# Kernel optimization log

Hardware: AMD Instinct MI355X
Metric: run time of the kernel (lower is better)

The kernel has to match this reference:

```python
import jax, jax.numpy as jnp
import numpy as np

N, E, L, F, HID, OUT = 20000, 200000, 5, 4, 128, 3


def _lin(x, w, b):
    # torch Linear convention: w is [out, in]
    return x @ w.T + b


def setup_inputs() -> dict:
    key = jax.random.key(0)
    ks = iter(jax.random.split(key, 40))
    nrm = lambda shape, s=0.05: jax.random.normal(next(ks), shape, dtype=jnp.float32) * s
    inp = {
        'x': jax.random.normal(next(ks), (N, L, F), dtype=jnp.float32),
        'edge_index': jax.random.randint(next(ks), (2, E), 0, N, dtype=jnp.int64),
        'edge_attr': jax.random.normal(next(ks), (E, F), dtype=jnp.float32),
        'batch': jnp.zeros((N,), dtype=jnp.int64),
        'node_type': jax.random.normal(next(ks), (N, 1), dtype=jnp.float32),
        # PastStateEncoder params
        'emb': nrm((L, F), 1.0),
        'conv_w': nrm((HID, 2 * F, 3)),  # Conv1d(8,128,3) OIW
        'conv_b': nrm((HID,)),
        # FusionLayer Linear(129,128)
        'fuse_w': nrm((HID, HID + 1)), 'fuse_b': nrm((HID,)),
        # gnn1 EdgeModel: Linear(2*128+4,128), Linear(128,128)
        'g1e_w1': nrm((HID, 2 * HID + F)), 'g1e_b1': nrm((HID,)),
        'g1e_w2': nrm((HID, HID)), 'g1e_b2': nrm((HID,)),
        # gnn1 NodeModel: Linear(256,128), Linear(128,128)
        'g1n_w1': nrm((HID, 2 * HID)), 'g1n_b1': nrm((HID,)),
        'g1n_w2': nrm((HID, HID)), 'g1n_b2': nrm((HID,)),
        # gnn2 EdgeModel: Linear(2*128+128,128), Linear(128,128)
        'g2e_w1': nrm((HID, 3 * HID)), 'g2e_b1': nrm((HID,)),
        'g2e_w2': nrm((HID, HID)), 'g2e_b2': nrm((HID,)),
        # gnn2 NodeModel
        'g2n_w1': nrm((HID, 2 * HID)), 'g2n_b1': nrm((HID,)),
        'g2n_w2': nrm((HID, HID)), 'g2n_b2': nrm((HID,)),
        # final_mlp: Linear(128,128), BN(128), Linear(128,3)
        'fm_w1': nrm((HID, HID)), 'fm_b1': nrm((HID,)),
        'bn_g': jnp.ones((HID,), dtype=jnp.float32), 'bn_b': jnp.zeros((HID,), dtype=jnp.float32),
        'fm_w2': nrm((OUT, HID)), 'fm_b2': nrm((OUT,)),
    }
    return inp


def _encoder(x, emb, conv_w, conv_b):
    # x: [N, L, F]; append learned positional embedding -> [N, L, 2F]
    n = x.shape[0]
    xe = jnp.concatenate([x, jnp.broadcast_to(emb[None], (n, L, F))], axis=-1)
    xc = xe.transpose(0, 2, 1)  # [N, 2F, L]
    y = jax.lax.conv_general_dilated(
        xc, conv_w, window_strides=(1,), padding=[(1, 1)],
        dimension_numbers=('NCW', 'OIW', 'NCW'))
    y = y + conv_b[None, :, None]
    return y.mean(axis=-1)  # [N, HID]


def _edge_mlp(src, dst, ea, w1, b1, w2, b2):
    h = jax.nn.relu(_lin(jnp.concatenate([src, dst, ea], axis=1), w1, b1))
    return _lin(h, w2, b2)


def _node_mlp(x_row, ea, w1, b1, w2, b2):
    h = jax.nn.relu(_lin(jnp.concatenate([x_row, ea], axis=1), w1, b1))
    return _lin(h, w2, b2)


def reference(x, edge_index, edge_attr, batch, node_type,
              emb, conv_w, conv_b, fuse_w, fuse_b,
              g1e_w1, g1e_b1, g1e_w2, g1e_b2, g1n_w1, g1n_b1, g1n_w2, g1n_b2,
              g2e_w1, g2e_b1, g2e_w2, g2e_b2, g2n_w1, g2n_b1, g2n_w2, g2n_b2,
              fm_w1, fm_b1, bn_g, bn_b, fm_w2, fm_b2):
    row, col = edge_index[0], edge_index[1]
    h = _encoder(x, emb, conv_w, conv_b)                     # [N,128]
    h = _lin(jnp.concatenate([h, node_type], axis=-1), fuse_w, fuse_b)  # [N,128]
    # gnn1 (MetaLayer: edge model then node model; node model here is per-edge)
    ea = _edge_mlp(h[row], h[col], edge_attr, g1e_w1, g1e_b1, g1e_w2, g1e_b2)  # [E,128]
    h = _node_mlp(h[row], ea, g1n_w1, g1n_b1, g1n_w2, g1n_b2)                  # [E,128]
    # gnn2 (h now lives on edges; indices < N <= E remain valid, matching torch)
    ea = _edge_mlp(h[row], h[col], ea, g2e_w1, g2e_b1, g2e_w2, g2e_b2)
    h = _node_mlp(h[row], ea, g2n_w1, g2n_b1, g2n_w2, g2n_b2)
    # final head on edge_attr: Linear -> BatchNorm1d (training stats) -> ReLU -> Linear
    z = _lin(ea, fm_w1, fm_b1)
    mu = z.mean(axis=0)
    var = z.var(axis=0)  # biased, matches torch BN normalization
    z = (z - mu) * jax.lax.rsqrt(var + 1e-5) * bn_g + bn_b
    z = jax.nn.relu(z)
    return _lin(z, fm_w2, fm_b2)  # [E,3]
```

## Files before the change

### kernel.cpp

```cpp
#include <hip/hip_runtime.h>

#define N_NODES 20000
#define N_EDGES 200000
#define HID 128
#define STR 136
#define NBLK 3125
#define NREP 64

typedef unsigned short u16;
using bf16x8 = __attribute__((ext_vector_type(8))) __bf16;
using f32x4  = __attribute__((ext_vector_type(4))) float;

__device__ __forceinline__ u16 f2bf(float f) {
  union { float f; unsigned u; } v; v.f = f;
  unsigned u = v.u;
  return (u16)((u + 0x7FFFu + ((u >> 16) & 1u)) >> 16);
}
__device__ __forceinline__ float bf2f(unsigned s) {
  union { unsigned u; float f; } v; v.u = s << 16;
  return v.f;
}
__device__ __forceinline__ bf16x8 ld8(const u16* p) { return *(const bf16x8*)p; }

__device__ __forceinline__ void zero_acc8(f32x4 acc[4]) {
#pragma unroll
  for (int i = 0; i < 4; ++i) acc[i] = (f32x4){0.f, 0.f, 0.f, 0.f};
}

template <int KSTEPS, typename AF>
__device__ __forceinline__ void wgemm8(const u16* __restrict__ PW, AF afrag,
                                       f32x4 acc[4], int lane, int wave) {
  const u16* pb = PW + (wave * 64 + lane) * 8;
  bf16x8 b[2];
  b[0] = ld8(pb);
#pragma unroll
  for (int ks = 0; ks < KSTEPS; ++ks) {
    const int cur = ks & 1;
    if (ks + 1 < KSTEPS) b[cur ^ 1] = ld8(pb + (ks + 1) * 4096);
#pragma unroll
    for (int mt = 0; mt < 4; ++mt) {
      bf16x8 a = afrag(ks, mt);
      acc[mt] = __builtin_amdgcn_mfma_f32_16x16x32_bf16(a, b[cur], acc[mt], 0, 0, 0);
    }
  }
}

template <bool RELU>
__device__ __forceinline__ void epi_store8(u16* buf, const f32x4 acc[4],
                                           const float* __restrict__ bias,
                                           int lane, int wave) {
  const int c = lane & 15, q = lane >> 4;
  const float bb = bias[wave * 16 + c];
  const int col = wave * 16 + c;
#pragma unroll
  for (int mt = 0; mt < 4; ++mt)
#pragma unroll
    for (int r = 0; r < 4; ++r) {
      float v = acc[mt][r] + bb;
      if (RELU) v = fmaxf(v, 0.f);
      buf[(mt * 16 + q * 4 + r) * STR + col] = f2bf(v);
    }
}

__device__ __forceinline__ void flush_buf8(const u16* buf, u16* __restrict__ gout,
                                           int e0, int tid) {
#pragma unroll
  for (int it = 0; it < 2; ++it) {
    int cid = tid + it * 512, e = cid >> 4, p = cid & 15;
    uint4 v = *(const uint4*)(buf + e * STR + p * 8);
    *(uint4*)(gout + (size_t)(e0 + e) * HID + p * 8) = v;
  }
}

__device__ __forceinline__ void stage_gather8(const int* __restrict__ rowI,
                                              const int* __restrict__ colI,
                                              const u16* __restrict__ htab,
                                              u16* B0, u16* B1,
                                              int e0, int lane, int wave) {
  const int r = lane >> 4, p = lane & 15;
#pragma unroll
  for (int it = 0; it < 4; ++it) {
    int j = wave * 16 + it * 4 + r;
    int e = j & 63;
    int id = (j < 64) ? rowI[e0 + e] : colI[e0 + e];
    uint4 v = *(const uint4*)(htab + (size_t)id * HID + p * 8);
    *(uint4*)(((j < 64) ? B0 : B1) + e * STR + p * 8) = v;
  }
}

__global__ __launch_bounds__(128) void k_prep1(
    const float* __restrict__ emb, const float* __restrict__ conv_w,
    const float* __restrict__ conv_b, const float* __restrict__ fuse_w,
    const float* __restrict__ fuse_b,
    const float* __restrict__ fm_w1, const float* __restrict__ g2e_b2,
    const float* __restrict__ fm_b1, const float* __restrict__ w6,
    float* __restrict__ Mt, float* __restrict__ C0, float* __restrict__ Wnt,
    float* __restrict__ b67, float* __restrict__ W67, float* __restrict__ bnrep) {
  __shared__ float red[22][129];
  __shared__ float w7s[128];
  const int o = blockIdx.x;
  const int j = threadIdx.x;
  bnrep[o * 128 + j] = 0.f;
  float A[21];
  {
    float b0 = conv_b[j];
#pragma unroll
    for (int p = 0; p < 5; ++p) {
#pragma unroll
      for (int i = 0; i < 8; ++i) {
        float s = 0.f;
#pragma unroll
        for (int k = 0; k < 3; ++k) {
          int t = p + 1 - k;
          if (t >= 0 && t < 5) s += conv_w[(j * 8 + i) * 3 + k];
        }
        s *= 0.2f;
        if (i < 4) A[p * 4 + i] = s;
        else b0 += emb[p * 4 + (i - 4)] * s;
      }
    }
    A[20] = b0;
  }
  float w = fuse_w[o * 129 + j];
  float w7 = fm_w1[o * 128 + j];
  w7s[j] = w7;
#pragma unroll
  for (int qq = 0; qq < 21; ++qq) red[qq][j] = w * A[qq];
  red[21][j] = w7 * g2e_b2[j];
  __syncthreads();
  if (j < 22) {
    float s = 0.f;
    for (int t = 0; t < 128; ++t) s += red[j][t];
    if (j < 20)      Mt[j * 128 + o] = s;
    else if (j == 20) C0[o] = s + fuse_b[o];
    else              b67[o] = s + fm_b1[o];
  }
  if (j == 0) Wnt[o] = fuse_w[o * 129 + 128];
  float s = 0.f;
  for (int t = 0; t < 128; ++t) s += w7s[t] * w6[t * 128 + j];
  W67[o * 128 + j] = s;
}

struct PackArgs {
  const float* src[6];
  u16* dst[6];
  int Kin[6];
  int ksCum[7];
};

__global__ __launch_bounds__(256) void k_prep2(
    PackArgs pa, const float* __restrict__ x, const float* __restrict__ node_type,
    const float* __restrict__ Mt, const float* __restrict__ C0,
    const float* __restrict__ Wnt, u16* __restrict__ h2) {
  if (blockIdx.x < 41) {
    int bk = blockIdx.x;
    int mi = 0;
    while (bk >= pa.ksCum[mi + 1]) ++mi;
    int ks = bk - pa.ksCum[mi];
    const float* W = pa.src[mi];
    u16* D = pa.dst[mi] + ks * 4096;
    int Kin = pa.Kin[mi];
#pragma unroll
    for (int t = 0; t < 16; ++t) {
      int el = t * 256 + (int)threadIdx.x;
      int j = el & 7, ln = (el >> 3) & 63, ntile = el >> 9;
      int k = ks * 32 + ((ln >> 4) << 3) + j;
      int n = ntile * 16 + (ln & 15);
      float v = (k < Kin) ? W[n * Kin + k] : 0.0f;
      D[el] = f2bf(v);
    }
    return;
  }
  __shared__ float xs[16][20], nts[16], mts[20 * 128];
  const int tid = threadIdx.x;
  const int n0 = ((int)blockIdx.x - 41) * 16;
  for (int i = tid; i < 320; i += 256) xs[i / 20][i % 20] = x[n0 * 20 + i];
  if (tid < 16) nts[tid] = node_type[n0 + tid];
  for (int i = tid; i < 2560; i += 256) mts[i] = Mt[i];
  __syncthreads();
  const int nl = tid >> 4;
  const int c0 = (tid & 15) * 8;
  float nt = nts[nl];
  union { u16 s[8]; uint4 u; } o;
#pragma unroll
  for (int i = 0; i < 8; ++i) {
    int ch = c0 + i;
    float acc = C0[ch] + Wnt[ch] * nt;
#pragma unroll
    for (int qq = 0; qq < 20; ++qq) acc += xs[nl][qq] * mts[qq * 128 + ch];
    o.s[i] = f2bf(acc);
  }
  *(uint4*)(h2 + (size_t)(n0 + nl) * HID + c0) = o.u;
}

__global__ __launch_bounds__(512, 8) void k_gnn1(
    const int* __restrict__ eidx, const float* __restrict__ eattr,
    const u16* __restrict__ h2, const u16* __restrict__ pW1, const u16* __restrict__ pW2,
    const u16* __restrict__ pW3, const u16* __restrict__ pW4, const float* __restrict__ b1,
    const float* __restrict__ b2, const float* __restrict__ b3, const float* __restrict__ b4,
    u16* __restrict__ ea1, u16* __restrict__ h3) {
  __shared__ __align__(16) u16 B0[64 * STR], B1[64 * STR];
  const int tid = threadIdx.x, lane = tid & 63, wave = tid >> 6;
  const int e0 = blockIdx.x * 64;
  const int m = lane & 15, q = lane >> 4;
  const int aoff = m * STR + q * 8;
  const int* rowI = eidx;
  const int* colI = eidx + N_EDGES;

  stage_gather8(rowI, colI, h2, B0, B1, e0, lane, wave);

  bf16x8 ef[4];
#pragma unroll
  for (int mt = 0; mt < 4; ++mt) {
    union { u16 s[8]; uint4 u; bf16x8 v; } t;
    t.u = make_uint4(0u, 0u, 0u, 0u);
    if (q == 0) {
      float4 a = *(const float4*)(eattr + (size_t)(e0 + mt * 16 + m) * 4);
      t.s[0] = f2bf(a.x); t.s[1] = f2bf(a.y); t.s[2] = f2bf(a.z); t.s[3] = f2bf(a.w);
    }
    ef[mt] = t.v;
  }
  __syncthreads();

  f32x4 acc[4];
  zero_acc8(acc);
  wgemm8<9>(pW1, [&](int ks, int mt) -> bf16x8 {
    if (ks < 4) return ld8(B0 + aoff + mt * 16 * STR + ks * 32);
    if (ks < 8) return ld8(B1 + aoff + mt * 16 * STR + (ks - 4) * 32);
    return ef[mt];
  }, acc, lane, wave);
  __syncthreads();
  epi_store8<true>(B1, acc, b1, lane, wave);
  __syncthreads();

  zero_acc8(acc);
  wgemm8<4>(pW2, [&](int ks, int mt) -> bf16x8 {
    return ld8(B1 + aoff + mt * 16 * STR + ks * 32);
  }, acc, lane, wave);
  epi_store8<false>(B0, acc, b2, lane, wave);
  __syncthreads();
  flush_buf8(B0, ea1, e0, tid);

  if (e0 < N_NODES) {
#pragma unroll
    for (int it = 0; it < 2; ++it) {
      int e = wave * 8 + it * 4 + q;
      int id = rowI[e0 + e];
      uint4 v = *(const uint4*)(h2 + (size_t)id * HID + m * 8);
      *(uint4*)(B1 + e * STR + m * 8) = v;
    }
    __syncthreads();

    zero_acc8(acc);
    wgemm8<8>(pW3, [&](int ks, int mt) -> bf16x8 {
      if (ks < 4) return ld8(B1 + aoff + mt * 16 * STR + ks * 32);
      return ld8(B0 + aoff + mt * 16 * STR + (ks - 4) * 32);
    }, acc, lane, wave);
    __syncthreads();
    epi_store8<true>(B1, acc, b3, lane, wave);
    __syncthreads();

    zero_acc8(acc);
    wgemm8<4>(pW4, [&](int ks, int mt) -> bf16x8 {
      return ld8(B1 + aoff + mt * 16 * STR + ks * 32);
    }, acc, lane, wave);
    epi_store8<false>(B0, acc, b4, lane, wave);
    __syncthreads();
    flush_buf8(B0, h3, e0, tid);
  }
}

__global__ __launch_bounds__(512, 8) void k_gnn2(
    const int* __restrict__ eidx, const u16* __restrict__ h3, u16* ea1z,
    const u16* __restrict__ pW5, const u16* __restrict__ pW67,
    const float* __restrict__ b5, const float* __restrict__ b67,
    float* __restrict__ bnrep) {
  __shared__ __align__(16) u16 B0[64 * STR], B1[64 * STR];
  const int tid = threadIdx.x, lane = tid & 63, wave = tid >> 6;
  const int e0 = blockIdx.x * 64;
  const int m = lane & 15, q = lane >> 4;
  const int aoff = m * STR + q * 8;
  const int* rowI = eidx;
  const int* colI = eidx + N_EDGES;

  stage_gather8(rowI, colI, h3, B0, B1, e0, lane, wave);
  __syncthreads();

  f32x4 acc[4];
  zero_acc8(acc);
  wgemm8<8>(pW5, [&](int ks, int mt) -> bf16x8 {
    if (ks < 4) return ld8(B0 + aoff + mt * 16 * STR + ks * 32);
    return ld8(B1 + aoff + mt * 16 * STR + (ks - 4) * 32);
  }, acc, lane, wave);
  __syncthreads();

#pragma unroll
  for (int it = 0; it < 2; ++it) {
    int cid = tid + it * 512, e = cid >> 4, p = cid & 15;
    uint4 v = *(const uint4*)(ea1z + (size_t)(e0 + e) * HID + p * 8);
    *(uint4*)(B0 + e * STR + p * 8) = v;
  }
  __syncthreads();

  wgemm8<4>(pW5 + 8 * 4096, [&](int ks, int mt) -> bf16x8 {
    return ld8(B0 + aoff + mt * 16 * STR + ks * 32);
  }, acc, lane, wave);
  epi_store8<true>(B1, acc, b5, lane, wave);
  __syncthreads();

  zero_acc8(acc);
  wgemm8<4>(pW67, [&](int ks, int mt) -> bf16x8 {
    return ld8(B1 + aoff + mt * 16 * STR + ks * 32);
  }, acc, lane, wave);

  {
    const int c = lane & 15;
    const int col = wave * 16 + c;
    const float bb = b67[col];
    float s0 = 0.f, q0 = 0.f;
#pragma unroll
    for (int mt = 0; mt < 4; ++mt)
#pragma unroll
      for (int r = 0; r < 4; ++r) {
        float v0 = acc[mt][r] + bb;
        s0 += v0; q0 += v0 * v0;
        int row = mt * 16 + q * 4 + r;
        B0[row * STR + col] = f2bf(v0);
      }
    s0 += __shfl_xor(s0, 16); s0 += __shfl_xor(s0, 32);
    q0 += __shfl_xor(q0, 16); q0 += __shfl_xor(q0, 32);
    if (lane < 16) {
      float* slot = bnrep + ((int)blockIdx.x & (NREP - 1)) * 256;
      atomicAdd(&slot[wave * 16 + lane], s0);
      atomicAdd(&slot[128 + wave * 16 + lane], q0);
    }
  }
  __syncthreads();
  flush_buf8(B0, ea1z, e0, tid);
}

__global__ __launch_bounds__(256) void k_head(const u16* __restrict__ z,
                                              const float* __restrict__ bnrep,
                                              const float* __restrict__ bn_g,
                                              const float* __restrict__ bn_b,
                                              const float* __restrict__ w2,
                                              const float* __restrict__ b2,
                                              float* __restrict__ out) {
  __shared__ float sh_s[128], sh_h[128], sh_w0[128], sh_w1[128], sh_w2[128];
  const int tid = threadIdx.x;
  {
    float s = 0.f;
    for (int r = 0; r < NREP; ++r) s += bnrep[r * 256 + tid];
    __shared__ float acc2[256];
    acc2[tid] = s;
    __syncthreads();
    if (tid < 128) {
      const float inv = 1.0f / (float)N_EDGES;
      float mu = acc2[tid] * inv;
      float var = acc2[128 + tid] * inv - mu * mu;
      float sc = bn_g[tid] * rsqrtf(var + 1e-5f);
      sh_s[tid] = sc;
      sh_h[tid] = bn_b[tid] - mu * sc;
      sh_w0[tid] = w2[tid];
      sh_w1[tid] = w2[128 + tid];
      sh_w2[tid] = w2[256 + tid];
    }
    __syncthreads();
  }
  const int lane = tid & 63, wave = tid >> 6;
  const int g = lane >> 4;
  const int p = lane & 15;
  const int c0 = p * 8;
  const float bb0 = b2[0], bb1 = b2[1], bb2 = b2[2];
#pragma unroll 4
  for (int it = 0; it < 16; ++it) {
    int e = (int)blockIdx.x * 256 + wave * 64 + it * 4 + g;
    if (e >= N_EDGES) break;
    uint4 v = *(const uint4*)(z + (size_t)e * HID + c0);
    unsigned wv[4] = {v.x, v.y, v.z, v.w};
    float a0 = 0.f, a1 = 0.f, a2 = 0.f;
#pragma unroll
    for (int k = 0; k < 4; ++k) {
      int ch = c0 + k * 2;
      float lo = bf2f(wv[k] & 0xffffu), hi = bf2f(wv[k] >> 16);
      float r0 = fmaxf(fmaf(lo, sh_s[ch], sh_h[ch]), 0.f);
      float r1 = fmaxf(fmaf(hi, sh_s[ch + 1], sh_h[ch + 1]), 0.f);
      a0 += r0 * sh_w0[ch] + r1 * sh_w0[ch + 1];
      a1 += r0 * sh_w1[ch] + r1 * sh_w1[ch + 1];
      a2 += r0 * sh_w2[ch] + r1 * sh_w2[ch + 1];
    }
#pragma unroll
    for (int off = 1; off < 16; off <<= 1) {
      a0 += __shfl_xor(a0, off);
      a1 += __shfl_xor(a1, off);
      a2 += __shfl_xor(a2, off);
    }
    if (p < 3) out[e * 3 + p] = (p == 0) ? a0 + bb0 : (p == 1) ? a1 + bb1 : a2 + bb2;
  }
}

extern "C" void kernel_launch(void* const* d_in, const int* in_sizes, int n_in,
                              void* d_out, int out_size, void* d_ws, size_t ws_size,
                              hipStream_t stream) {
  const float* x         = (const float*)d_in[0];
  const int* eidx        = (const int*)d_in[1];
  const float* eattr     = (const float*)d_in[2];
  const float* node_type = (const float*)d_in[4];
  const float* emb       = (const float*)d_in[5];
  const float* conv_w    = (const float*)d_in[6];
  const float* conv_b    = (const float*)d_in[7];
  const float* fuse_w    = (const float*)d_in[8];
  const float* fuse_b    = (const float*)d_in[9];
  const float* g1e_w1    = (const float*)d_in[10];
  const float* g1e_b1    = (const float*)d_in[11];
  const float* g1e_w2    = (const float*)d_in[12];
  const float* g1e_b2    = (const float*)d_in[13];
  const float* g1n_w1    = (const float*)d_in[14];
  const float* g1n_b1    = (const float*)d_in[15];
  const float* g1n_w2    = (const float*)d_in[16];
  const float* g1n_b2    = (const float*)d_in[17];
  const float* g2e_w1    = (const float*)d_in[18];
  const float* g2e_b1    = (const float*)d_in[19];
  const float* g2e_w2    = (const float*)d_in[20];
  const float* g2e_b2    = (const float*)d_in[21];
  const float* fm_w1     = (const float*)d_in[26];
  const float* fm_b1     = (const float*)d_in[27];
  const float* bn_g      = (const float*)d_in[28];
  const float* bn_b      = (const float*)d_in[29];
  const float* fm_w2     = (const float*)d_in[30];
  const float* fm_b2     = (const float*)d_in[31];
  float* out = (float*)d_out;

  char* ws = (char*)d_ws;
  size_t off = 0;
  auto take = [&](size_t bytes) {
    void* p = ws + off;
    off = (off + bytes + 255) & ~(size_t)255;
    return p;
  };
  u16* h2   = (u16*)take((size_t)N_NODES * HID * 2);
  u16* h3   = (u16*)take((size_t)20032 * HID * 2);
  u16* ea1z = (u16*)take((size_t)N_EDGES * HID * 2);
  float* Mt    = (float*)take(20 * 128 * 4);
  float* C0    = (float*)take(128 * 4);
  float* Wnt   = (float*)take(128 * 4);
  float* b67   = (float*)take(128 * 4);
  float* W67f  = (float*)take(128 * 128 * 4);
  float* bnrep = (float*)take((size_t)NREP * 256 * 4);
  u16* pW1  = (u16*)take(9 * 4096 * 2);
  u16* pW2  = (u16*)take(4 * 4096 * 2);
  u16* pW3  = (u16*)take(8 * 4096 * 2);
  u16* pW4  = (u16*)take(4 * 4096 * 2);
  u16* pW5  = (u16*)take(12 * 4096 * 2);
  u16* pW67 = (u16*)take(4 * 4096 * 2);

  k_prep1<<<128, 128, 0, stream>>>(emb, conv_w, conv_b, fuse_w, fuse_b,
                                   fm_w1, g2e_b2, fm_b1, g2e_w2,
                                   Mt, C0, Wnt, b67, W67f, bnrep);

  PackArgs pa;
  const float* srcs[6] = {g1e_w1, g1e_w2, g1n_w1, g1n_w2, g2e_w1, W67f};
  u16* dsts[6] = {pW1, pW2, pW3, pW4, pW5, pW67};
  int kins[6] = {260, 128, 256, 128, 384, 128};
  int kst[6] = {9, 4, 8, 4, 12, 4};
  int cum = 0;
  for (int i = 0; i < 6; ++i) {
    pa.src[i] = srcs[i]; pa.dst[i] = dsts[i]; pa.Kin[i] = kins[i];
    pa.ksCum[i] = cum; cum += kst[i];
  }
  pa.ksCum[6] = cum;

  k_prep2<<<41 + N_NODES / 16, 256, 0, stream>>>(pa, x, node_type, Mt, C0, Wnt, h2);
  k_gnn1<<<NBLK, 512, 0, stream>>>(eidx, eattr, h2, pW1, pW2, pW3, pW4,
                                   g1e_b1, g1e_b2, g1n_b1, g1n_b2, ea1z, h3);
  k_gnn2<<<NBLK, 512, 0, stream>>>(eidx, h3, ea1z, pW5, pW67,
                                   g2e_b1, b67, bnrep);
  k_head<<<(N_EDGES + 255) / 256, 256, 0, stream>>>(ea1z, bnrep, bn_g, bn_b,
                                                    fm_w2, fm_b2, out);
}
```

Measured before the change: 232.4 us.

## Precompute per-node linear projections before gathering onto edges

Splits the first-layer weights of the edge and node MLPs by input segment, so the row and column halves are applied once per node in new k_pre/k_pre2 kernels instead of once per edge. The edge kernels then gather the projected node rows and add them, with the 4-wide edge_attr term done in scalar FMAs. This removes most of the K=256/384 per-edge GEMM work in exchange for two extra launches, extra workspace, and extra bf16 rounding of the intermediate projections. Launch bounds change from 8 to 4 waves.

```diff
diff --git a/kernel.cpp b/kernel.cpp
--- a/kernel.cpp
+++ b/kernel.cpp
@@ -5,6 +5,7 @@
 #define HID 128
 #define STR 136
 #define NBLK 3125
+#define NPRE 313
 #define NREP 64
 
 typedef unsigned short u16;
@@ -62,6 +63,36 @@
     }
 }
 
+template <bool RELU>
+__device__ __forceinline__ void epi_add8(u16* out, const u16* addb,
+                                         const f32x4 acc[4],
+                                         const float* __restrict__ bias,
+                                         int lane, int wave) {
+  const int c = lane & 15, q = lane >> 4;
+  const int col = wave * 16 + c;
+  const float bb = bias[col];
+#pragma unroll
+  for (int mt = 0; mt < 4; ++mt)
+#pragma unroll
+    for (int r = 0; r < 4; ++r) {
+      int row = mt * 16 + q * 4 + r;
+      float v = acc[mt][r] + bf2f(addb[row * STR + col]) + bb;
+      if (RELU) v = fmaxf(v, 0.f);
+      out[row * STR + col] = f2bf(v);
+    }
+}
+
+__device__ __forceinline__ void epi_plain8(u16* buf, const f32x4 acc[4],
+                                           int lane, int wave) {
+  const int c = lane & 15, q = lane >> 4;
+  const int col = wave * 16 + c;
+#pragma unroll
+  for (int mt = 0; mt < 4; ++mt)
+#pragma unroll
+    for (int r = 0; r < 4; ++r)
+      buf[(mt * 16 + q * 4 + r) * STR + col] = f2bf(acc[mt][r]);
+}
+
 __device__ __forceinline__ void flush_buf8(const u16* buf, u16* __restrict__ gout,
                                            int e0, int tid) {
 #pragma unroll
@@ -69,22 +100,6 @@
     int cid = tid + it * 512, e = cid >> 4, p = cid & 15;
     uint4 v = *(const uint4*)(buf + e * STR + p * 8);
     *(uint4*)(gout + (size_t)(e0 + e) * HID + p * 8) = v;
-  }
-}
-
-__device__ __forceinline__ void stage_gather8(const int* __restrict__ rowI,
-                                              const int* __restrict__ colI,
-                                              const u16* __restrict__ htab,
-                                              u16* B0, u16* B1,
-                                              int e0, int lane, int wave) {
-  const int r = lane >> 4, p = lane & 15;
-#pragma unroll
-  for (int it = 0; it < 4; ++it) {
-    int j = wave * 16 + it * 4 + r;
-    int e = j & 63;
-    int id = (j < 64) ? rowI[e0 + e] : colI[e0 + e];
-    uint4 v = *(const uint4*)(htab + (size_t)id * HID + p * 8);
-    *(uint4*)(((j < 64) ? B0 : B1) + e * STR + p * 8) = v;
   }
 }
 
@@ -142,38 +157,34 @@
 }
 
 struct PackArgs {
-  const float* src[6];
-  u16* dst[6];
-  int Kin[6];
-  int ksCum[7];
+  const float* src[10];
+  u16* dst[10];
+  int stride[10];
+  int koff[10];
 };
 
 __global__ __launch_bounds__(256) void k_prep2(
     PackArgs pa, const float* __restrict__ x, const float* __restrict__ node_type,
     const float* __restrict__ Mt, const float* __restrict__ C0,
     const float* __restrict__ Wnt, u16* __restrict__ h2) {
-  if (blockIdx.x < 41) {
-    int bk = blockIdx.x;
-    int mi = 0;
-    while (bk >= pa.ksCum[mi + 1]) ++mi;
-    int ks = bk - pa.ksCum[mi];
+  if (blockIdx.x < 40) {
+    int mi = blockIdx.x >> 2, ks = blockIdx.x & 3;
     const float* W = pa.src[mi];
     u16* D = pa.dst[mi] + ks * 4096;
-    int Kin = pa.Kin[mi];
+    const int stride = pa.stride[mi], koff = pa.koff[mi];
 #pragma unroll
     for (int t = 0; t < 16; ++t) {
       int el = t * 256 + (int)threadIdx.x;
       int j = el & 7, ln = (el >> 3) & 63, ntile = el >> 9;
       int k = ks * 32 + ((ln >> 4) << 3) + j;
       int n = ntile * 16 + (ln & 15);
-      float v = (k < Kin) ? W[n * Kin + k] : 0.0f;
-      D[el] = f2bf(v);
+      D[el] = f2bf(W[n * stride + koff + k]);
     }
     return;
   }
   __shared__ float xs[16][20], nts[16], mts[20 * 128];
   const int tid = threadIdx.x;
-  const int n0 = ((int)blockIdx.x - 41) * 16;
+  const int n0 = ((int)blockIdx.x - 40) * 16;
   for (int i = tid; i < 320; i += 256) xs[i / 20][i % 20] = x[n0 * 20 + i];
   if (tid < 16) nts[tid] = node_type[n0 + tid];
   for (int i = tid; i < 2560; i += 256) mts[i] = Mt[i];
@@ -193,71 +204,134 @@
   *(uint4*)(h2 + (size_t)(n0 + nl) * HID + c0) = o.u;
 }
 
-__global__ __launch_bounds__(512, 8) void k_gnn1(
+__device__ __forceinline__ void dense_pass(const u16* __restrict__ pW,
+                                           u16* B0, u16* B1,
+                                           u16* __restrict__ outT, int n0,
+                                           int tid, int lane, int wave, int aoff) {
+  f32x4 acc[4];
+  zero_acc8(acc);
+  wgemm8<4>(pW, [&](int ks, int mt) -> bf16x8 {
+    return ld8(B0 + aoff + mt * 16 * STR + ks * 32);
+  }, acc, lane, wave);
+  __syncthreads();
+  epi_plain8(B1, acc, lane, wave);
+  __syncthreads();
+  flush_buf8(B1, outT, n0, tid);
+}
+
+__global__ __launch_bounds__(512, 4) void k_pre(
+    const u16* __restrict__ h2, const u16* __restrict__ pW1a,
+    const u16* __restrict__ pW1b, const u16* __restrict__ pW3a,
+    u16* __restrict__ ut, u16* __restrict__ vt, u16* __restrict__ wt) {
+  __shared__ __align__(16) u16 B0[64 * STR], B1[64 * STR];
+  const int tid = threadIdx.x, lane = tid & 63, wave = tid >> 6;
+  const int n0 = blockIdx.x * 64;
+  const int aoff = (lane & 15) * STR + (lane >> 4) * 8;
+#pragma unroll
+  for (int it = 0; it < 2; ++it) {
+    int cid = tid + it * 512, r = cid >> 4, p = cid & 15;
+    int n = min(n0 + r, N_NODES - 1);
+    uint4 v = *(const uint4*)(h2 + (size_t)n * HID + p * 8);
+    *(uint4*)(B0 + r * STR + p * 8) = v;
+  }
+  __syncthreads();
+  dense_pass(pW1a, B0, B1, ut, n0, tid, lane, wave, aoff);
+  dense_pass(pW1b, B0, B1, vt, n0, tid, lane, wave, aoff);
+  dense_pass(pW3a, B0, B1, wt, n0, tid, lane, wave, aoff);
+}
+
+__global__ __launch_bounds__(512, 4) void k_pre2(
+    const u16* __restrict__ h3, const u16* __restrict__ pW5a,
+    const u16* __restrict__ pW5b,
+    u16* __restrict__ zat, u16* __restrict__ zbt) {
+  __shared__ __align__(16) u16 B0[64 * STR], B1[64 * STR];
+  const int tid = threadIdx.x, lane = tid & 63, wave = tid >> 6;
+  const int n0 = blockIdx.x * 64;
+  const int aoff = (lane & 15) * STR + (lane >> 4) * 8;
+#pragma unroll
+  for (int it = 0; it < 2; ++it) {
+    int cid = tid + it * 512, r = cid >> 4, p = cid & 15;
+    uint4 v = *(const uint4*)(h3 + (size_t)(n0 + r) * HID + p * 8);
+    *(uint4*)(B0 + r * STR + p * 8) = v;
+  }
+  __syncthreads();
+  dense_pass(pW5a, B0, B1, zat, n0, tid, lane, wave, aoff);
+  dense_pass(pW5b, B0, B1, zbt, n0, tid, lane, wave, aoff);
+}
+
+__global__ __launch_bounds__(512, 4) void k_gnn1(
     const int* __restrict__ eidx, const float* __restrict__ eattr,
-    const u16* __restrict__ h2, const u16* __restrict__ pW1, const u16* __restrict__ pW2,
-    const u16* __restrict__ pW3, const u16* __restrict__ pW4, const float* __restrict__ b1,
-    const float* __restrict__ b2, const float* __restrict__ b3, const float* __restrict__ b4,
+    const float* __restrict__ g1e_w1,
+    const u16* __restrict__ ut, const u16* __restrict__ vt, const u16* __restrict__ wt,
+    const u16* __restrict__ pW2, const u16* __restrict__ pW3b, const u16* __restrict__ pW4,
+    const float* __restrict__ b1, const float* __restrict__ b2,
+    const float* __restrict__ b3, const float* __restrict__ b4,
     u16* __restrict__ ea1, u16* __restrict__ h3) {
   __shared__ __align__(16) u16 B0[64 * STR], B1[64 * STR];
   const int tid = threadIdx.x, lane = tid & 63, wave = tid >> 6;
   const int e0 = blockIdx.x * 64;
-  const int m = lane & 15, q = lane >> 4;
-  const int aoff = m * STR + q * 8;
+  const int aoff = (lane & 15) * STR + (lane >> 4) * 8;
   const int* rowI = eidx;
   const int* colI = eidx + N_EDGES;
 
-  stage_gather8(rowI, colI, h2, B0, B1, e0, lane, wave);
-
-  bf16x8 ef[4];
-#pragma unroll
-  for (int mt = 0; mt < 4; ++mt) {
-    union { u16 s[8]; uint4 u; bf16x8 v; } t;
-    t.u = make_uint4(0u, 0u, 0u, 0u);
-    if (q == 0) {
-      float4 a = *(const float4*)(eattr + (size_t)(e0 + mt * 16 + m) * 4);
-      t.s[0] = f2bf(a.x); t.s[1] = f2bf(a.y); t.s[2] = f2bf(a.z); t.s[3] = f2bf(a.w);
-    }
-    ef[mt] = t.v;
+  {
+    const int p = tid & 15, ch0 = p * 8;
+    float4 wc0 = *(const float4*)(g1e_w1 + (ch0 + 0) * 260 + 256);
+    float4 wc1 = *(const float4*)(g1e_w1 + (ch0 + 1) * 260 + 256);
+    float4 wc2 = *(const float4*)(g1e_w1 + (ch0 + 2) * 260 + 256);
+    float4 wc3 = *(const float4*)(g1e_w1 + (ch0 + 3) * 260 + 256);
+    float4 wc4 = *(const float4*)(g1e_w1 + (ch0 + 4) * 260 + 256);
+    float4 wc5 = *(const float4*)(g1e_w1 + (ch0 + 5) * 260 + 256);
+    float4 wc6 = *(const float4*)(g1e_w1 + (ch0 + 6) * 260 + 256);
+    float4 wc7 = *(const float4*)(g1e_w1 + (ch0 + 7) * 260 + 256);
+    float4 bA = *(const float4*)(b1 + ch0);
+    float4 bB = *(const float4*)(b1 + ch0 + 4);
+    const float bb[8] = {bA.x, bA.y, bA.z, bA.w, bB.x, bB.y, bB.z, bB.w};
+#pragma unroll
+    for (int it = 0; it < 2; ++it) {
+      int e = (tid >> 4) + it * 32;
+      int row = rowI[e0 + e], col = colI[e0 + e];
+      union { uint4 q; u16 s[8]; } U, V, O;
+      U.q = *(const uint4*)(ut + (size_t)row * HID + ch0);
+      V.q = *(const uint4*)(vt + (size_t)col * HID + ch0);
+      float4 ea = *(const float4*)(eattr + (size_t)(e0 + e) * 4);
+      const float4 wc[8] = {wc0, wc1, wc2, wc3, wc4, wc5, wc6, wc7};
+#pragma unroll
+      for (int i = 0; i < 8; ++i) {
+        float c = ea.x * wc[i].x + ea.y * wc[i].y + ea.z * wc[i].z + ea.w * wc[i].w;
+        float val = bf2f(U.s[i]) + bf2f(V.s[i]) + c + bb[i];
+        O.s[i] = f2bf(fmaxf(val, 0.f));
+      }
+      *(uint4*)(B0 + e * STR + p * 8) = O.q;
+    }
   }
   __syncthreads();
 
   f32x4 acc[4];
   zero_acc8(acc);
-  wgemm8<9>(pW1, [&](int ks, int mt) -> bf16x8 {
-    if (ks < 4) return ld8(B0 + aoff + mt * 16 * STR + ks * 32);
-    if (ks < 8) return ld8(B1 + aoff + mt * 16 * STR + (ks - 4) * 32);
-    return ef[mt];
+  wgemm8<4>(pW2, [&](int ks, int mt) -> bf16x8 {
+    return ld8(B0 + aoff + mt * 16 * STR + ks * 32);
   }, acc, lane, wave);
-  __syncthreads();
-  epi_store8<true>(B1, acc, b1, lane, wave);
-  __syncthreads();
-
-  zero_acc8(acc);
-  wgemm8<4>(pW2, [&](int ks, int mt) -> bf16x8 {
-    return ld8(B1 + aoff + mt * 16 * STR + ks * 32);
-  }, acc, lane, wave);
-  epi_store8<false>(B0, acc, b2, lane, wave);
-  __syncthreads();
-  flush_buf8(B0, ea1, e0, tid);
+  epi_store8<false>(B1, acc, b2, lane, wave);
+  __syncthreads();
+  flush_buf8(B1, ea1, e0, tid);
 
   if (e0 < N_NODES) {
 #pragma unroll
     for (int it = 0; it < 2; ++it) {
-      int e = wave * 8 + it * 4 + q;
+      int cid = tid + it * 512, e = cid >> 4, p = cid & 15;
       int id = rowI[e0 + e];
-      uint4 v = *(const uint4*)(h2 + (size_t)id * HID + m * 8);
-      *(uint4*)(B1 + e * STR + m * 8) = v;
+      uint4 v = *(const uint4*)(wt + (size_t)id * HID + p * 8);
+      *(uint4*)(B0 + e * STR + p * 8) = v;
     }
     __syncthreads();
 
     zero_acc8(acc);
-    wgemm8<8>(pW3, [&](int ks, int mt) -> bf16x8 {
-      if (ks < 4) return ld8(B1 + aoff + mt * 16 * STR + ks * 32);
-      return ld8(B0 + aoff + mt * 16 * STR + (ks - 4) * 32);
+    wgemm8<4>(pW3b, [&](int ks, int mt) -> bf16x8 {
+      return ld8(B1 + aoff + mt * 16 * STR + ks * 32);
     }, acc, lane, wave);
     __syncthreads();
-    epi_store8<true>(B1, acc, b3, lane, wave);
+    epi_add8<true>(B1, B0, acc, b3, lane, wave);
     __syncthreads();
 
     zero_acc8(acc);
@@ -270,9 +344,10 @@
   }
 }
 
-__global__ __launch_bounds__(512, 8) void k_gnn2(
-    const int* __restrict__ eidx, const u16* __restrict__ h3, u16* ea1z,
-    const u16* __restrict__ pW5, const u16* __restrict__ pW67,
+__global__ __launch_bounds__(512, 4) void k_gnn2(
+    const int* __restrict__ eidx,
+    const u16* __restrict__ zat, const u16* __restrict__ zbt, u16* ea1z,
+    const u16* __restrict__ pW5c, const u16* __restrict__ pW67,
     const float* __restrict__ b5, const float* __restrict__ b67,
     float* __restrict__ bnrep) {
   __shared__ __align__(16) u16 B0[64 * STR], B1[64 * STR];
@@ -283,29 +358,28 @@
   const int* rowI = eidx;
   const int* colI = eidx + N_EDGES;
 
-  stage_gather8(rowI, colI, h3, B0, B1, e0, lane, wave);
+#pragma unroll
+  for (int it = 0; it < 2; ++it) {
+    int cid = tid + it * 512, e = cid >> 4, p = cid & 15;
+    int row = rowI[e0 + e], col = colI[e0 + e];
+    union { uint4 q; u16 s[8]; } A, B, O;
+    A.q = *(const uint4*)(zat + (size_t)row * HID + p * 8);
+    B.q = *(const uint4*)(zbt + (size_t)col * HID + p * 8);
+#pragma unroll
+    for (int i = 0; i < 8; ++i) O.s[i] = f2bf(bf2f(A.s[i]) + bf2f(B.s[i]));
+    *(uint4*)(B1 + e * STR + p * 8) = O.q;
+    uint4 z = *(const uint4*)(ea1z + (size_t)(e0 + e) * HID + p * 8);
+    *(uint4*)(B0 + e * STR + p * 8) = z;
+  }
   __syncthreads();
 
   f32x4 acc[4];
   zero_acc8(acc);
-  wgemm8<8>(pW5, [&](int ks, int mt) -> bf16x8 {
-    if (ks < 4) return ld8(B0 + aoff + mt * 16 * STR + ks * 32);
-    return ld8(B1 + aoff + mt * 16 * STR + (ks - 4) * 32);
-  }, acc, lane, wave);
-  __syncthreads();
-
-#pragma unroll
-  for (int it = 0; it < 2; ++it) {
-    int cid = tid + it * 512, e = cid >> 4, p = cid & 15;
-    uint4 v = *(const uint4*)(ea1z + (size_t)(e0 + e) * HID + p * 8);
-    *(uint4*)(B0 + e * STR + p * 8) = v;
-  }
-  __syncthreads();
-
-  wgemm8<4>(pW5 + 8 * 4096, [&](int ks, int mt) -> bf16x8 {
+  wgemm8<4>(pW5c, [&](int ks, int mt) -> bf16x8 {
     return ld8(B0 + aoff + mt * 16 * STR + ks * 32);
   }, acc, lane, wave);
-  epi_store8<true>(B1, acc, b5, lane, wave);
+  __syncthreads();
+  epi_add8<true>(B1, B1, acc, b5, lane, wave);
   __syncthreads();
 
   zero_acc8(acc);
@@ -441,17 +515,26 @@
   u16* h2   = (u16*)take((size_t)N_NODES * HID * 2);
   u16* h3   = (u16*)take((size_t)20032 * HID * 2);
   u16* ea1z = (u16*)take((size_t)N_EDGES * HID * 2);
+  u16* ut   = (u16*)take((size_t)20032 * HID * 2);
+  u16* vt   = (u16*)take((size_t)20032 * HID * 2);
+  u16* wt   = (u16*)take((size_t)20032 * HID * 2);
+  u16* zat  = (u16*)take((size_t)20032 * HID * 2);
+  u16* zbt  = (u16*)take((size_t)20032 * HID * 2);
   float* Mt    = (float*)take(20 * 128 * 4);
   float* C0    = (float*)take(128 * 4);
   float* Wnt   = (float*)take(128 * 4);
   float* b67   = (float*)take(128 * 4);
   float* W67f  = (float*)take(128 * 128 * 4);
   float* bnrep = (float*)take((size_t)NREP * 256 * 4);
-  u16* pW1  = (u16*)take(9 * 4096 * 2);
+  u16* pW1a = (u16*)take(4 * 4096 * 2);
+  u16* pW1b = (u16*)take(4 * 4096 * 2);
+  u16* pW3a = (u16*)take(4 * 4096 * 2);
+  u16* pW3b = (u16*)take(4 * 4096 * 2);
   u16* pW2  = (u16*)take(4 * 4096 * 2);
-  u16* pW3  = (u16*)take(8 * 4096 * 2);
   u16* pW4  = (u16*)take(4 * 4096 * 2);
-  u16* pW5  = (u16*)take(12 * 4096 * 2);
+  u16* pW5a = (u16*)take(4 * 4096 * 2);
+  u16* pW5b = (u16*)take(4 * 4096 * 2);
+  u16* pW5c = (u16*)take(4 * 4096 * 2);
   u16* pW67 = (u16*)take(4 * 4096 * 2);
 
   k_prep1<<<128, 128, 0, stream>>>(emb, conv_w, conv_b, fuse_w, fuse_b,
@@ -459,21 +542,23 @@
                                    Mt, C0, Wnt, b67, W67f, bnrep);
 
   PackArgs pa;
-  const float* srcs[6] = {g1e_w1, g1e_w2, g1n_w1, g1n_w2, g2e_w1, W67f};
-  u16* dsts[6] = {pW1, pW2, pW3, pW4, pW5, pW67};
-  int kins[6] = {260, 128, 256, 128, 384, 128};
-  int kst[6] = {9, 4, 8, 4, 12, 4};
-  int cum = 0;
-  for (int i = 0; i < 6; ++i) {
-    pa.src[i] = srcs[i]; pa.dst[i] = dsts[i]; pa.Kin[i] = kins[i];
-    pa.ksCum[i] = cum; cum += kst[i];
-  }
-  pa.ksCum[6] = cum;
-
-  k_prep2<<<41 + N_NODES / 16, 256, 0, stream>>>(pa, x, node_type, Mt, C0, Wnt, h2);
-  k_gnn1<<<NBLK, 512, 0, stream>>>(eidx, eattr, h2, pW1, pW2, pW3, pW4,
+  const float* srcs[10] = {g1e_w1, g1e_w1, g1n_w1, g1n_w1, g1e_w2,
+                           g1n_w2, g2e_w1, g2e_w1, g2e_w1, W67f};
+  u16* dsts[10] = {pW1a, pW1b, pW3a, pW3b, pW2, pW4, pW5a, pW5b, pW5c, pW67};
+  int strd[10] = {260, 260, 256, 256, 128, 128, 384, 384, 384, 128};
+  int kofs[10] = {0, 128, 0, 128, 0, 0, 0, 128, 256, 0};
+  for (int i = 0; i < 10; ++i) {
+    pa.src[i] = srcs[i]; pa.dst[i] = dsts[i];
+    pa.stride[i] = strd[i]; pa.koff[i] = kofs[i];
+  }
+
+  k_prep2<<<40 + N_NODES / 16, 256, 0, stream>>>(pa, x, node_type, Mt, C0, Wnt, h2);
+  k_pre<<<NPRE, 512, 0, stream>>>(h2, pW1a, pW1b, pW3a, ut, vt, wt);
+  k_gnn1<<<NBLK, 512, 0, stream>>>(eidx, eattr, g1e_w1, ut, vt, wt,
+                                   pW2, pW3b, pW4,
                                    g1e_b1, g1e_b2, g1n_b1, g1n_b2, ea1z, h3);
-  k_gnn2<<<NBLK, 512, 0, stream>>>(eidx, h3, ea1z, pW5, pW67,
+  k_pre2<<<NPRE, 512, 0, stream>>>(h3, pW5a, pW5b, zat, zbt);
+  k_gnn2<<<NBLK, 512, 0, stream>>>(eidx, zat, zbt, ea1z, pW5c, pW67,
                                    g2e_b1, b67, bnrep);
   k_head<<<(N_EDGES + 255) / 256, 256, 0, stream>>>(ea1z, bnrep, bn_g, bn_b,
                                                     fm_w2, fm_b2, out);
```

Measured after the change: 255.7 us. 1.1x slower.

## Process two edge tiles per block and prefetch second tile's gathers during first

Applied to the files above, without the earlier changes.

Each GNN block now handles two 64-edge tiles. The second tile's index reads and h/ea gathers are issued into registers before the first tile's GEMM chain, so global gather latency overlaps with MFMA work. Barriers use a custom LDS-only waitcnt plus s_barrier, and the gnn1 node-model path reuses the already-staged row features instead of regathering them. Launch bounds drop to 4 waves per SIMD to leave room for the extra prefetch registers, which lowers occupancy and halves the grid.

```diff
diff --git a/kernel.cpp b/kernel.cpp
--- a/kernel.cpp
+++ b/kernel.cpp
@@ -4,7 +4,7 @@
 #define N_EDGES 200000
 #define HID 128
 #define STR 136
-#define NBLK 3125
+#define NBLKG 1563
 #define NREP 64
 
 typedef unsigned short u16;
@@ -21,6 +21,12 @@
   return v.f;
 }
 __device__ __forceinline__ bf16x8 ld8(const u16* p) { return *(const bf16x8*)p; }
+
+__device__ __forceinline__ void bar_lds() {
+  asm volatile("s_waitcnt lgkmcnt(0)" ::: "memory");
+  __builtin_amdgcn_s_barrier();
+  asm volatile("" ::: "memory");
+}
 
 __device__ __forceinline__ void zero_acc8(f32x4 acc[4]) {
 #pragma unroll
@@ -85,6 +91,20 @@
     int id = (j < 64) ? rowI[e0 + e] : colI[e0 + e];
     uint4 v = *(const uint4*)(htab + (size_t)id * HID + p * 8);
     *(uint4*)(((j < 64) ? B0 : B1) + e * STR + p * 8) = v;
+  }
+}
+
+__device__ __forceinline__ void make_ef(bf16x8 ef[4], const float* __restrict__ eattr,
+                                        int e0, int m, int q) {
+#pragma unroll
+  for (int mt = 0; mt < 4; ++mt) {
+    union { u16 s[8]; uint4 u; bf16x8 v; } t;
+    t.u = make_uint4(0u, 0u, 0u, 0u);
+    if (q == 0) {
+      float4 a = *(const float4*)(eattr + (size_t)(e0 + mt * 16 + m) * 4);
+      t.s[0] = f2bf(a.x); t.s[1] = f2bf(a.y); t.s[2] = f2bf(a.z); t.s[3] = f2bf(a.w);
+    }
+    ef[mt] = t.v;
   }
 }
 
@@ -193,7 +213,54 @@
   *(uint4*)(h2 + (size_t)(n0 + nl) * HID + c0) = o.u;
 }
 
-__global__ __launch_bounds__(512, 8) void k_gnn1(
+template <typename H1>
+__device__ __forceinline__ void gnn1_chain(
+    u16* B0, u16* B1, const bf16x8 ef[4],
+    const u16* __restrict__ pW1, const u16* __restrict__ pW2,
+    const u16* __restrict__ pW3, const u16* __restrict__ pW4,
+    const float* __restrict__ b1, const float* __restrict__ b2,
+    const float* __restrict__ b3, const float* __restrict__ b4,
+    u16* __restrict__ ea1, u16* __restrict__ h3,
+    int e0, int tid, int lane, int wave, int aoff, H1 issue) {
+  f32x4 acc[4];
+  zero_acc8(acc);
+  issue();
+  wgemm8<9>(pW1, [&](int ks, int mt) -> bf16x8 {
+    if (ks < 4) return ld8(B0 + aoff + mt * 16 * STR + ks * 32);
+    if (ks < 8) return ld8(B1 + aoff + mt * 16 * STR + (ks - 4) * 32);
+    return ef[mt];
+  }, acc, lane, wave);
+  bar_lds();
+  epi_store8<true>(B1, acc, b1, lane, wave);
+  bar_lds();
+  zero_acc8(acc);
+  wgemm8<4>(pW2, [&](int ks, int mt) -> bf16x8 {
+    return ld8(B1 + aoff + mt * 16 * STR + ks * 32);
+  }, acc, lane, wave);
+  bar_lds();
+  epi_store8<false>(B1, acc, b2, lane, wave);
+  bar_lds();
+  flush_buf8(B1, ea1, e0, tid);
+  if (e0 < N_NODES) {
+    zero_acc8(acc);
+    wgemm8<8>(pW3, [&](int ks, int mt) -> bf16x8 {
+      if (ks < 4) return ld8(B0 + aoff + mt * 16 * STR + ks * 32);
+      return ld8(B1 + aoff + mt * 16 * STR + (ks - 4) * 32);
+    }, acc, lane, wave);
+    bar_lds();
+    epi_store8<true>(B1, acc, b3, lane, wave);
+    bar_lds();
+    zero_acc8(acc);
+    wgemm8<4>(pW4, [&](int ks, int mt) -> bf16x8 {
+      return ld8(B1 + aoff + mt * 16 * STR + ks * 32);
+    }, acc, lane, wave);
+    epi_store8<false>(B0, acc, b4, lane, wave);
+    bar_lds();
+    flush_buf8(B0, h3, e0, tid);
+  }
+}
+
+__global__ __launch_bounds__(512, 4) void k_gnn1(
     const int* __restrict__ eidx, const float* __restrict__ eattr,
     const u16* __restrict__ h2, const u16* __restrict__ pW1, const u16* __restrict__ pW2,
     const u16* __restrict__ pW3, const u16* __restrict__ pW4, const float* __restrict__ b1,
@@ -201,118 +268,80 @@
     u16* __restrict__ ea1, u16* __restrict__ h3) {
   __shared__ __align__(16) u16 B0[64 * STR], B1[64 * STR];
   const int tid = threadIdx.x, lane = tid & 63, wave = tid >> 6;
-  const int e0 = blockIdx.x * 64;
+  const int e0 = (int)blockIdx.x * 128;
+  const int e1 = e0 + 64;
+  const bool hasB = (e1 < N_EDGES);
   const int m = lane & 15, q = lane >> 4;
   const int aoff = m * STR + q * 8;
   const int* rowI = eidx;
   const int* colI = eidx + N_EDGES;
+  const int jr = lane >> 4, jp = lane & 15;
+  const int j0 = wave * 16 + jr, j1 = j0 + 4, j2 = j0 + 8, j3 = j0 + 12;
 
   stage_gather8(rowI, colI, h2, B0, B1, e0, lane, wave);
-
   bf16x8 ef[4];
-#pragma unroll
-  for (int mt = 0; mt < 4; ++mt) {
-    union { u16 s[8]; uint4 u; bf16x8 v; } t;
-    t.u = make_uint4(0u, 0u, 0u, 0u);
-    if (q == 0) {
-      float4 a = *(const float4*)(eattr + (size_t)(e0 + mt * 16 + m) * 4);
-      t.s[0] = f2bf(a.x); t.s[1] = f2bf(a.y); t.s[2] = f2bf(a.z); t.s[3] = f2bf(a.w);
-    }
-    ef[mt] = t.v;
-  }
-  __syncthreads();
-
+  make_ef(ef, eattr, e0, m, q);
+  int i0 = 0, i1 = 0, i2 = 0, i3 = 0;
+  if (hasB) {
+    i0 = ((j0 < 64) ? rowI : colI)[e1 + (j0 & 63)];
+    i1 = ((j1 < 64) ? rowI : colI)[e1 + (j1 & 63)];
+    i2 = ((j2 < 64) ? rowI : colI)[e1 + (j2 & 63)];
+    i3 = ((j3 < 64) ? rowI : colI)[e1 + (j3 & 63)];
+  }
+  bar_lds();
+
+  uint4 g0, g1, g2, g3;
+  gnn1_chain(B0, B1, ef, pW1, pW2, pW3, pW4, b1, b2, b3, b4,
+             ea1, h3, e0, tid, lane, wave, aoff, [&]() {
+    if (hasB) {
+      g0 = *(const uint4*)(h2 + (size_t)i0 * HID + jp * 8);
+      g1 = *(const uint4*)(h2 + (size_t)i1 * HID + jp * 8);
+      g2 = *(const uint4*)(h2 + (size_t)i2 * HID + jp * 8);
+      g3 = *(const uint4*)(h2 + (size_t)i3 * HID + jp * 8);
+    }
+  });
+
+  if (hasB) {
+    bar_lds();
+    *(uint4*)(((j0 < 64) ? B0 : B1) + (j0 & 63) * STR + jp * 8) = g0;
+    *(uint4*)(((j1 < 64) ? B0 : B1) + (j1 & 63) * STR + jp * 8) = g1;
+    *(uint4*)(((j2 < 64) ? B0 : B1) + (j2 & 63) * STR + jp * 8) = g2;
+    *(uint4*)(((j3 < 64) ? B0 : B1) + (j3 & 63) * STR + jp * 8) = g3;
+    bf16x8 efB[4];
+    make_ef(efB, eattr, e1, m, q);
+    bar_lds();
+    gnn1_chain(B0, B1, efB, pW1, pW2, pW3, pW4, b1, b2, b3, b4,
+               ea1, h3, e1, tid, lane, wave, aoff, []() {});
+  }
+}
+
+template <typename H1, typename SZ>
+__device__ __forceinline__ void gnn2_chain(
+    u16* B0, u16* B1,
+    const u16* __restrict__ pW5, const u16* __restrict__ pW67,
+    const float* __restrict__ b5, const float* __restrict__ b67,
+    float* __restrict__ bnrep, u16* __restrict__ ea1z, int e0, int slot,
+    int tid, int lane, int wave, int aoff, H1 issue, SZ stageZ) {
+  const int q = lane >> 4;
   f32x4 acc[4];
   zero_acc8(acc);
-  wgemm8<9>(pW1, [&](int ks, int mt) -> bf16x8 {
-    if (ks < 4) return ld8(B0 + aoff + mt * 16 * STR + ks * 32);
-    if (ks < 8) return ld8(B1 + aoff + mt * 16 * STR + (ks - 4) * 32);
-    return ef[mt];
-  }, acc, lane, wave);
-  __syncthreads();
-  epi_store8<true>(B1, acc, b1, lane, wave);
-  __syncthreads();
-
-  zero_acc8(acc);
-  wgemm8<4>(pW2, [&](int ks, int mt) -> bf16x8 {
-    return ld8(B1 + aoff + mt * 16 * STR + ks * 32);
-  }, acc, lane, wave);
-  epi_store8<false>(B0, acc, b2, lane, wave);
-  __syncthreads();
-  flush_buf8(B0, ea1, e0, tid);
-
-  if (e0 < N_NODES) {
-#pragma unroll
-    for (int it = 0; it < 2; ++it) {
-      int e = wave * 8 + it * 4 + q;
-      int id = rowI[e0 + e];
-      uint4 v = *(const uint4*)(h2 + (size_t)id * HID + m * 8);
-      *(uint4*)(B1 + e * STR + m * 8) = v;
-    }
-    __syncthreads();
-
-    zero_acc8(acc);
-    wgemm8<8>(pW3, [&](int ks, int mt) -> bf16x8 {
-      if (ks < 4) return ld8(B1 + aoff + mt * 16 * STR + ks * 32);
-      return ld8(B0 + aoff + mt * 16 * STR + (ks - 4) * 32);
-    }, acc, lane, wave);
-    __syncthreads();
-    epi_store8<true>(B1, acc, b3, lane, wave);
-    __syncthreads();
-
-    zero_acc8(acc);
-    wgemm8<4>(pW4, [&](int ks, int mt) -> bf16x8 {
-      return ld8(B1 + aoff + mt * 16 * STR + ks * 32);
-    }, acc, lane, wave);
-    epi_store8<false>(B0, acc, b4, lane, wave);
-    __syncthreads();
-    flush_buf8(B0, h3, e0, tid);
-  }
-}
-
-__global__ __launch_bounds__(512, 8) void k_gnn2(
-    const int* __restrict__ eidx, const u16* __restrict__ h3, u16* ea1z,
-    const u16* __restrict__ pW5, const u16* __restrict__ pW67,
-    const float* __restrict__ b5, const float* __restrict__ b67,
-    float* __restrict__ bnrep) {
-  __shared__ __align__(16) u16 B0[64 * STR], B1[64 * STR];
-  const int tid = threadIdx.x, lane = tid & 63, wave = tid >> 6;
-  const int e0 = blockIdx.x * 64;
-  const int m = lane & 15, q = lane >> 4;
-  const int aoff = m * STR + q * 8;
-  const int* rowI = eidx;
-  const int* colI = eidx + N_EDGES;
-
-  stage_gather8(rowI, colI, h3, B0, B1, e0, lane, wave);
-  __syncthreads();
-
-  f32x4 acc[4];
-  zero_acc8(acc);
+  issue();
   wgemm8<8>(pW5, [&](int ks, int mt) -> bf16x8 {
     if (ks < 4) return ld8(B0 + aoff + mt * 16 * STR + ks * 32);
     return ld8(B1 + aoff + mt * 16 * STR + (ks - 4) * 32);
   }, acc, lane, wave);
-  __syncthreads();
-
-#pragma unroll
-  for (int it = 0; it < 2; ++it) {
-    int cid = tid + it * 512, e = cid >> 4, p = cid & 15;
-    uint4 v = *(const uint4*)(ea1z + (size_t)(e0 + e) * HID + p * 8);
-    *(uint4*)(B0 + e * STR + p * 8) = v;
-  }
-  __syncthreads();
-
+  bar_lds();
+  stageZ();
+  bar_lds();
   wgemm8<4>(pW5 + 8 * 4096, [&](int ks, int mt) -> bf16x8 {
     return ld8(B0 + aoff + mt * 16 * STR + ks * 32);
   }, acc, lane, wave);
   epi_store8<true>(B1, acc, b5, lane, wave);
-  __syncthreads();
-
+  bar_lds();
   zero_acc8(acc);
   wgemm8<4>(pW67, [&](int ks, int mt) -> bf16x8 {
     return ld8(B1 + aoff + mt * 16 * STR + ks * 32);
   }, acc, lane, wave);
-
   {
     const int c = lane & 15;
     const int col = wave * 16 + c;
@@ -330,13 +359,80 @@
     s0 += __shfl_xor(s0, 16); s0 += __shfl_xor(s0, 32);
     q0 += __shfl_xor(q0, 16); q0 += __shfl_xor(q0, 32);
     if (lane < 16) {
-      float* slot = bnrep + ((int)blockIdx.x & (NREP - 1)) * 256;
-      atomicAdd(&slot[wave * 16 + lane], s0);
-      atomicAdd(&slot[128 + wave * 16 + lane], q0);
-    }
-  }
-  __syncthreads();
+      float* sl = bnrep + slot * 256;
+      atomicAdd(&sl[wave * 16 + lane], s0);
+      atomicAdd(&sl[128 + wave * 16 + lane], q0);
+    }
+  }
+  bar_lds();
   flush_buf8(B0, ea1z, e0, tid);
+}
+
+__global__ __launch_bounds__(512, 4) void k_gnn2(
+    const int* __restrict__ eidx, const u16* __restrict__ h3, u16* ea1z,
+    const u16* __restrict__ pW5, const u16* __restrict__ pW67,
+    const float* __restrict__ b5, const float* __restrict__ b67,
+    float* __restrict__ bnrep) {
+  __shared__ __align__(16) u16 B0[64 * STR], B1[64 * STR];
+  const int tid = threadIdx.x, lane = tid & 63, wave = tid >> 6;
+  const int e0 = (int)blockIdx.x * 128;
+  const int e1 = e0 + 64;
+  const bool hasB = (e1 < N_EDGES);
+  const int m = lane & 15, q = lane >> 4;
+  const int aoff = m * STR + q * 8;
+  const int* rowI = eidx;
+  const int* colI = eidx + N_EDGES;
+  const int jr = lane >> 4, jp = lane & 15;
+  const int j0 = wave * 16 + jr, j1 = j0 + 4, j2 = j0 + 8, j3 = j0 + 12;
+  const int ez = tid >> 4, pz = tid & 15;
+
+  stage_gather8(rowI, colI, h3, B0, B1, e0, lane, wave);
+  int i0 = 0, i1 = 0, i2 = 0, i3 = 0;
+  if (hasB) {
+    i0 = ((j0 < 64) ? rowI : colI)[e1 + (j0 & 63)];
+    i1 = ((j1 < 64) ? rowI : colI)[e1 + (j1 & 63)];
+    i2 = ((j2 < 64) ? rowI : colI)[e1 + (j2 & 63)];
+    i3 = ((j3 < 64) ? rowI : colI)[e1 + (j3 & 63)];
+  }
+  bar_lds();
+
+  uint4 g0, g1, g2, g3, za, zb;
+  gnn2_chain(B0, B1, pW5, pW67, b5, b67, bnrep, ea1z, e0,
+             (2 * (int)blockIdx.x) & (NREP - 1), tid, lane, wave, aoff,
+    [&]() {
+      if (hasB) {
+        g0 = *(const uint4*)(h3 + (size_t)i0 * HID + jp * 8);
+        g1 = *(const uint4*)(h3 + (size_t)i1 * HID + jp * 8);
+        g2 = *(const uint4*)(h3 + (size_t)i2 * HID + jp * 8);
+        g3 = *(const uint4*)(h3 + (size_t)i3 * HID + jp * 8);
+        za = *(const uint4*)(ea1z + (size_t)(e1 + ez) * HID + pz * 8);
+        zb = *(const uint4*)(ea1z + (size_t)(e1 + 32 + ez) * HID + pz * 8);
+      }
+    },
+    [&]() {
+#pragma unroll
+      for (int it = 0; it < 2; ++it) {
+        int cid = tid + it * 512, e = cid >> 4, p = cid & 15;
+        uint4 v = *(const uint4*)(ea1z + (size_t)(e0 + e) * HID + p * 8);
+        *(uint4*)(B0 + e * STR + p * 8) = v;
+      }
+    });
+
+  if (hasB) {
+    bar_lds();
+    *(uint4*)(((j0 < 64) ? B0 : B1) + (j0 & 63) * STR + jp * 8) = g0;
+    *(uint4*)(((j1 < 64) ? B0 : B1) + (j1 & 63) * STR + jp * 8) = g1;
+    *(uint4*)(((j2 < 64) ? B0 : B1) + (j2 & 63) * STR + jp * 8) = g2;
+    *(uint4*)(((j3 < 64) ? B0 : B1) + (j3 & 63) * STR + jp * 8) = g3;
+    bar_lds();
+    gnn2_chain(B0, B1, pW5, pW67, b5, b67, bnrep, ea1z, e1,
+               (2 * (int)blockIdx.x + 1) & (NREP - 1), tid, lane, wave, aoff,
+      []() {},
+      [&]() {
+        *(uint4*)(B0 + ez * STR + pz * 8) = za;
+        *(uint4*)(B0 + (32 + ez) * STR + pz * 8) = zb;
+      });
+  }
 }
 
 __global__ __launch_bounds__(256) void k_head(const u16* __restrict__ z,
@@ -471,10 +567,10 @@
   pa.ksCum[6] = cum;
 
   k_prep2<<<41 + N_NODES / 16, 256, 0, stream>>>(pa, x, node_type, Mt, C0, Wnt, h2);
-  k_gnn1<<<NBLK, 512, 0, stream>>>(eidx, eattr, h2, pW1, pW2, pW3, pW4,
-                                   g1e_b1, g1e_b2, g1n_b1, g1n_b2, ea1z, h3);
-  k_gnn2<<<NBLK, 512, 0, stream>>>(eidx, h3, ea1z, pW5, pW67,
-                                   g2e_b1, b67, bnrep);
+  k_gnn1<<<NBLKG, 512, 0, stream>>>(eidx, eattr, h2, pW1, pW2, pW3, pW4,
+                                    g1e_b1, g1e_b2, g1n_b1, g1n_b2, ea1z, h3);
+  k_gnn2<<<NBLKG, 512, 0, stream>>>(eidx, h3, ea1z, pW5, pW67,
+                                    g2e_b1, b67, bnrep);
   k_head<<<(N_EDGES + 255) / 256, 256, 0, stream>>>(ea1z, bnrep, bn_g, bn_b,
                                                     fm_w2, fm_b2, out);
 }
```

New measurement: 251.4 us. +8.2%, slower.
